# Performance work log

Measured on AMD Instinct MI355X. Metric: run time of the kernel, lower is better.

The kernel has to match this reference:

```python
import jax, jax.numpy as jnp
import numpy as np

B, T, ENC_IN, DEC_IN, U = 32768, 7, 60, 36, 356


def setup_inputs() -> dict:
    key = jax.random.key(0)
    ks = jax.random.split(key, 12)
    s = 0.05  # small weight scale for numerical sanity
    return {
        "x_batch": jax.random.normal(ks[0], (B, T, ENC_IN), jnp.float32),
        "m_batch": jax.random.normal(ks[1], (B, T, DEC_IN), jnp.float32),
        "enc_kernel": jax.random.normal(ks[2], (ENC_IN, 4 * U), jnp.float32) * s,
        "enc_rec_kernel": jax.random.normal(ks[3], (U, 4 * U), jnp.float32) * s,
        "enc_bias": jnp.zeros((4 * U,), jnp.float32),
        "dec_kernel": jax.random.normal(ks[4], (DEC_IN, 4 * U), jnp.float32) * s,
        "dec_rec_kernel": jax.random.normal(ks[5], (U, 4 * U), jnp.float32) * s,
        "dec_bias": jnp.zeros((4 * U,), jnp.float32),
        "W_map": jax.random.normal(ks[6], (T * U, 768), jnp.float32) * s,
        "b_map": jnp.zeros((768,), jnp.float32),
        "W_deep1": jax.random.normal(ks[7], (768, 768), jnp.float32) * s,
        "b_deep1": jnp.zeros((768,), jnp.float32),
        "W_deep2": jax.random.normal(ks[8], (768, 768), jnp.float32) * s,
        "b_deep2": jnp.zeros((768,), jnp.float32),
        "W_out": jax.random.normal(ks[9], (768, 168), jnp.float32) * s,
        "b_out": jnp.zeros((168,), jnp.float32),
    }


def _lstm(x, K, R, b, h0, c0):
    """Keras-style LSTM. x: [B,T,D]. Returns (hs [B,T,U], h_T, c_T).
    Gate order i, f, g(candidate), o; sigmoid recurrent activation, tanh activation."""
    xz = jnp.einsum('btd,dg->btg', x, K) + b  # precompute input projections [B,T,4U]

    def step(carry, xz_t):
        h, c = carry
        z = xz_t + h @ R
        i, f, g, o = jnp.split(z, 4, axis=-1)
        c = jax.nn.sigmoid(f) * c + jax.nn.sigmoid(i) * jnp.tanh(g)
        h = jax.nn.sigmoid(o) * jnp.tanh(c)
        return (h, c), h

    (h, c), hs = jax.lax.scan(step, (h0, c0), jnp.swapaxes(xz, 0, 1))
    return jnp.swapaxes(hs, 0, 1), h, c


def reference(x_batch, m_batch, enc_kernel, enc_rec_kernel, enc_bias,
              dec_kernel, dec_rec_kernel, dec_bias,
              W_map, b_map, W_deep1, b_deep1, W_deep2, b_deep2, W_out, b_out):
    b = x_batch.shape[0]
    z = jnp.zeros((b, U), x_batch.dtype)
    # encoder: only final states used
    _, s_h, s_c = _lstm(x_batch, enc_kernel, enc_rec_kernel, enc_bias, z, z)
    # decoder: full sequence, initialized with encoder states
    decoded, _, _ = _lstm(m_batch, dec_kernel, dec_rec_kernel, dec_bias, s_h, s_c)
    f = decoded.reshape(b, -1)  # [B, 7*356]
    m = jax.nn.relu(f @ W_map + b_map)
    d = jnp.tanh(m @ W_deep1 + b_deep1)
    d = jnp.tanh(d @ W_deep2 + b_deep2)
    return d @ W_out + b_out
```

## Files before the change

kernel.cpp:

```cpp
#include <hip/hip_runtime.h>

typedef unsigned short u16;
typedef __attribute__((ext_vector_type(8))) short short8;
typedef __attribute__((ext_vector_type(4))) float f32x4;

#define B_ROWS 32768
#define T_STEPS 7
#define ENC_INd 60
#define DEC_INd 36
#define UNITS 356
#define KP_LSTM 448
#define H_OFF 64
#define HID 768
#define OUTN 168
#define OUTNP 256
#define KMAP 2688
#define HALF_E 44040192ull
#define WLSTM_E 688128

__device__ __forceinline__ u16 f2b(float f) {
  unsigned u = __builtin_bit_cast(unsigned, f);
  u += 0x7fffu + ((u >> 16) & 1u);
  return (u16)(u >> 16);
}
__device__ __forceinline__ float sigm(float x) { return 1.0f / (1.0f + __expf(-x)); }
__device__ __forceinline__ float tanhfast(float x) { return 2.0f / (1.0f + __expf(-2.0f * x)) - 1.0f; }

__global__ void fill_sentinel(float* __restrict__ out, int n, float v) {
  int i = blockIdx.x * 256 + threadIdx.x;
  int stride = gridDim.x * 256;
  for (; i < n; i += stride) out[i] = v;
}

__global__ void prep_lstm_w(const float* __restrict__ Km, const float* __restrict__ Rm,
                            const float* __restrict__ bias, int in_dim,
                            u16* __restrict__ WT, float* __restrict__ bias_r)
{
  int idx = blockIdx.x * 256 + threadIdx.x;
  if (idx >= WLSTM_E) return;
  int e    = idx & 7;
  int lane = (idx >> 3) & 63;
  int nf   = (idx >> 9) & 3;
  int t1   = idx >> 11;
  int kk   = t1 % 14;
  int g    = t1 / 14;
  int u = g * 16 + (lane & 15);
  int k = kk * 32 + ((lane >> 4) << 3) + e;
  float v = 0.f;
  if (u < UNITS) {
    int oc = nf * UNITS + u;
    if (k < in_dim) v = Km[(size_t)k * 1424 + oc];
    else if (k >= H_OFF && k < H_OFF + UNITS) v = Rm[(size_t)(k - H_OFF) * 1424 + oc];
    if (k == 0) bias_r[(u << 2) + nf] = bias[oc];
  } else if (k == 0) bias_r[(u << 2) + nf] = 0.f;
  WT[idx] = f2b(v);
}

__global__ void prep_map_w(const float* __restrict__ W, u16* __restrict__ WT)
{
  int idx = blockIdx.x * 256 + threadIdx.x;
  if (idx >= HID * KMAP) return;
  int n = idx / KMAP, k = idx - n * KMAP;
  int t = k / 384, kk = k - t * 384;
  float v = (kk < UNITS) ? W[(size_t)(t * UNITS + kk) * HID + n] : 0.f;
  WT[idx] = f2b(v);
}

__global__ void prep_mlp_w(const float* __restrict__ W, int korig, int norig, int kp,
                           u16* __restrict__ WT, int total)
{
  int idx = blockIdx.x * 256 + threadIdx.x;
  if (idx >= total) return;
  int n = idx / kp, k = idx - n * kp;
  float v = (k < korig && n < norig) ? W[(size_t)k * norig + n] : 0.f;
  WT[idx] = f2b(v);
}

__global__ __launch_bounds__(512)
void lstm_persistent(const float* __restrict__ xg, const float* __restrict__ mg,
                     const u16* __restrict__ WTe, const float* __restrict__ bre,
                     const u16* __restrict__ WTd, const float* __restrict__ brd,
                     u16* __restrict__ fbuf)
{
  __shared__ __align__(16) u16 A[32][KP_LSTM];

  const int tid = threadIdx.x;
  const int ns = tid >> 6;
  const int lane = tid & 63;
  const int l15 = lane & 15, l4 = lane >> 4;
  const int row0 = blockIdx.x * 32;

  float    c_reg[3][2][4];
  unsigned h_pack[3][2][2];
#pragma unroll
  for (int a = 0; a < 3; ++a)
#pragma unroll
    for (int b = 0; b < 2; ++b) {
      c_reg[a][b][0] = c_reg[a][b][1] = c_reg[a][b][2] = c_reg[a][b][3] = 0.f;
      h_pack[a][b][0] = 0u; h_pack[a][b][1] = 0u;
    }

#pragma unroll 1
  for (int s = 0; s < 14; ++s) {
    const u16*  wt = (s < 7) ? WTe : WTd;
    const float* br = (s < 7) ? bre : brd;
    const float* src = (s < 7) ? xg : mg;
    const int in_dim = (s < 7) ? ENC_INd : DEC_INd;
    const int t = (s < 7) ? s : s - 7;

    __syncthreads();

#pragma unroll
    for (int p = 0; p < 3; ++p) {
      const int g = p * 8 + ns;
      const int c = H_OFF + (g << 4) + l15;
      const int cb = c >> 3, ci = c & 7;
#pragma unroll
      for (int mf = 0; mf < 2; ++mf)
#pragma unroll
        for (int r = 0; r < 4; ++r) {
          const int row = (mf << 4) + (l4 << 2) + r;
          const int cbs = (cb & 56) | ((cb ^ row) & 7);
          unsigned pk = h_pack[p][mf][r >> 1];
          A[row][(cbs << 3) + ci] = (u16)((r & 1) ? (pk >> 16) : (pk & 0xffffu));
        }
    }
    if (tid < 256) {
      const int row = tid >> 3, cb = tid & 7;
      const float* sp = src + ((size_t)(row0 + row) * T_STEPS + t) * in_dim;
      const int cbs = cb ^ (row & 7);
      short8 vv;
#pragma unroll
      for (int j = 0; j < 8; ++j) {
        const int cc = (cb << 3) + j;
        float v = (cc < in_dim) ? sp[cc] : 0.f;
        vv[j] = (short)f2b(v);
      }
      *(short8*)&A[row][cbs << 3] = vv;
    }
    __syncthreads();

#pragma unroll 1
    for (int p = 0; p < 3; ++p) {
      const int g = p * 8 + ns;
      f32x4 acc[2][4] = {};
      const u16* bp = wt + ((size_t)g * 14) * 2048 + (lane << 3);

#pragma unroll 2
      for (int kk = 0; kk < 14; ++kk) {
        short8 af[2], bf[4];
#pragma unroll
        for (int mf = 0; mf < 2; ++mf) {
          const int ra = (mf << 4) + l15;
          const int cbA = (kk << 2) + l4;
          const int cbs = (cbA & 56) | ((cbA ^ ra) & 7);
          af[mf] = *(const short8*)&A[ra][cbs << 3];
        }
#pragma unroll
        for (int nf = 0; nf < 4; ++nf)
          bf[nf] = *(const short8*)(bp + kk * 2048 + (nf << 9));
#pragma unroll
        for (int mf = 0; mf < 2; ++mf)
#pragma unroll
          for (int nf = 0; nf < 4; ++nf)
            acc[mf][nf] = __builtin_amdgcn_mfma_f32_16x16x32_bf16(af[mf], bf[nf], acc[mf][nf], 0, 0, 0);
      }

      const int u = (g << 4) + l15;
      float bz[4];
#pragma unroll
      for (int nf = 0; nf < 4; ++nf) bz[nf] = br[(u << 2) + nf];
#pragma unroll
      for (int mf = 0; mf < 2; ++mf)
#pragma unroll
        for (int r = 0; r < 4; ++r) {
          const int row = (mf << 4) + (l4 << 2) + r;
          float zi = acc[mf][0][r] + bz[0];
          float zf = acc[mf][1][r] + bz[1];
          float zg = acc[mf][2][r] + bz[2];
          float zo = acc[mf][3][r] + bz[3];
          float ig = sigm(zi), fg = sigm(zf);
          float gg = tanhfast(zg), og = sigm(zo);
          float cn = fg * c_reg[p][mf][r] + ig * gg;
          c_reg[p][mf][r] = cn;
          float hv = og * tanhfast(cn);
          u16 hb = f2b(hv);
          unsigned& hp = h_pack[p][mf][r >> 1];
          if (r & 1) hp = (hp & 0xffffu) | ((unsigned)hb << 16);
          else       hp = (hp & 0xffff0000u) | (unsigned)hb;
          if (s >= 7) {
            const int grow = row0 + row;
            fbuf[(size_t)(grow >> 14) * HALF_E
                 + ((size_t)(grow & 16383) * T_STEPS + t) * 384 + u] = hb;
          }
        }
    }
  }
}

template<int MODE>
__global__ __launch_bounds__(256)
void mlp_gemm(const u16* __restrict__ A, int lda, int kp,
              const u16* __restrict__ WT, const float* __restrict__ bias, int nreal,
              u16* __restrict__ outb, float* __restrict__ outf, int ldo)
{
  __shared__ __align__(16) u16 lds_a[128 * 64];
  __shared__ __align__(16) u16 lds_b[128 * 64];
  const int tid = threadIdx.x;
  const int wid = tid >> 6, lane = tid & 63;
  const int wm = (wid >> 1) << 6, wn = (wid & 1) << 6;
  const int l15 = lane & 15, l4 = lane >> 4;
  const int r0 = tid >> 3, c8 = tid & 7;
  const size_t abase = (size_t)blockIdx.x * 128 * lda;
  const size_t bbase = (size_t)blockIdx.y * 128 * kp;

  f32x4 acc[4][4] = {};

  for (int kt = 0; kt < kp; kt += 64) {
#pragma unroll
    for (int p = 0; p < 4; ++p) {
      int r = r0 + p * 32;
      short8 va = *(const short8*)(A + abase + (size_t)r * lda + kt + (c8 << 3));
      *(short8*)&lds_a[(r << 6) + ((c8 ^ (r & 7)) << 3)] = va;
      short8 vb = *(const short8*)(WT + bbase + (size_t)r * kp + kt + (c8 << 3));
      *(short8*)&lds_b[(r << 6) + ((c8 ^ (r & 7)) << 3)] = vb;
    }
    __syncthreads();
#pragma unroll
    for (int kk = 0; kk < 2; ++kk) {
      short8 af[4], bfr[4];
#pragma unroll
      for (int mf = 0; mf < 4; ++mf) {
        int ra = wm + (mf << 4) + l15;
        int cb = (kk << 2) + l4;
        af[mf] = *(const short8*)&lds_a[(ra << 6) + ((cb ^ (ra & 7)) << 3)];
      }
#pragma unroll
      for (int nf = 0; nf < 4; ++nf) {
        int rb = wn + (nf << 4) + l15;
        int cb = (kk << 2) + l4;
        bfr[nf] = *(const short8*)&lds_b[(rb << 6) + ((cb ^ (rb & 7)) << 3)];
      }
#pragma unroll
      for (int mf = 0; mf < 4; ++mf)
#pragma unroll
        for (int nf = 0; nf < 4; ++nf)
          acc[mf][nf] = __builtin_amdgcn_mfma_f32_16x16x32_bf16(af[mf], bfr[nf], acc[mf][nf], 0, 0, 0);
    }
    __syncthreads();
  }

#pragma unroll
  for (int mf = 0; mf < 4; ++mf) {
    int rowb = blockIdx.x * 128 + wm + (mf << 4) + (l4 << 2);
#pragma unroll
    for (int r = 0; r < 4; ++r) {
      int row = rowb + r;
#pragma unroll
      for (int nf = 0; nf < 4; ++nf) {
        int n = blockIdx.y * 128 + wn + (nf << 4) + l15;
        float v = acc[mf][nf][r];
        size_t oi = (size_t)row * ldo + n;
        if (MODE == 3) {
          outb[oi] = f2b(tanhfast(v + bias[n]));
        } else if (MODE == 5) {
          outb[oi] = f2b(fmaxf(v + bias[n], 0.f));
        } else {
          if (n < nreal) outf[oi] = v + bias[n];
        }
      }
    }
  }
}

extern "C" void kernel_launch(void* const* d_in, const int* in_sizes, int n_in,
                              void* d_out, int out_size, void* d_ws, size_t ws_size,
                              hipStream_t stream)
{
  const float* x    = (const float*)d_in[0];
  const float* m    = (const float*)d_in[1];
  const float* ek   = (const float*)d_in[2];
  const float* erk  = (const float*)d_in[3];
  const float* eb   = (const float*)d_in[4];
  const float* dk   = (const float*)d_in[5];
  const float* drk  = (const float*)d_in[6];
  const float* dbi  = (const float*)d_in[7];
  const float* wmap = (const float*)d_in[8];
  const float* bmap = (const float*)d_in[9];
  const float* wd1  = (const float*)d_in[10];
  const float* bd1  = (const float*)d_in[11];
  const float* wd2  = (const float*)d_in[12];
  const float* bd2  = (const float*)d_in[13];
  const float* wout = (const float*)d_in[14];
  const float* bout = (const float*)d_in[15];

  char* ws = (char*)d_ws;
  size_t off = 0;
  auto alloc = [&](size_t bytes) { char* p = ws + off; off += (bytes + 255) & ~(size_t)255; return p; };

  u16*   WT_enc  = (u16*)  alloc((size_t)WLSTM_E * 2);
  u16*   WT_dec  = (u16*)  alloc((size_t)WLSTM_E * 2);
  float* b_enc_r = (float*)alloc((size_t)384 * 4 * 4);
  float* b_dec_r = (float*)alloc((size_t)384 * 4 * 4);
  u16*   WT_map  = (u16*)  alloc((size_t)HID * KMAP * 2);
  u16*   WT_d1   = (u16*)  alloc((size_t)HID * HID * 2);
  u16*   WT_d2   = (u16*)  alloc((size_t)HID * HID * 2);
  u16*   WT_out  = (u16*)  alloc((size_t)OUTNP * HID * 2);
  u16*   m1_h1   = (u16*)  alloc((size_t)16384 * HID * 2);
  u16*   fbuf    = (u16*)  alloc((size_t)2 * HALF_E * 2);
  const size_t NEED = off;

  if (ws_size < NEED) {
    fill_sentinel<<<256, 256, 0, stream>>>((float*)d_out, out_size, (float)(ws_size >> 20));
    return;
  }

  u16* fb_h0 = fbuf;
  u16* fb_h1 = fbuf + HALF_E;
  u16* m1_h0 = fb_h1;
  u16* m2_h0 = fb_h0;
  u16* m2_h1 = fb_h0 + (size_t)16384 * HID;
  u16* m3_h0 = fb_h1;
  u16* m3_h1 = m1_h1;

  prep_lstm_w<<<(WLSTM_E + 255) / 256, 256, 0, stream>>>(ek, erk, eb, ENC_INd, WT_enc, b_enc_r);
  prep_lstm_w<<<(WLSTM_E + 255) / 256, 256, 0, stream>>>(dk, drk, dbi, DEC_INd, WT_dec, b_dec_r);
  prep_map_w<<<((HID * KMAP) + 255) / 256, 256, 0, stream>>>(wmap, WT_map);
  prep_mlp_w<<<((HID * HID) + 255) / 256, 256, 0, stream>>>(wd1, HID, HID, HID, WT_d1, HID * HID);
  prep_mlp_w<<<((HID * HID) + 255) / 256, 256, 0, stream>>>(wd2, HID, HID, HID, WT_d2, HID * HID);
  prep_mlp_w<<<((OUTNP * HID) + 255) / 256, 256, 0, stream>>>(wout, HID, OUTN, HID, WT_out, OUTNP * HID);

  lstm_persistent<<<1024, 512, 0, stream>>>(x, m, WT_enc, b_enc_r, WT_dec, b_dec_r, fbuf);

  mlp_gemm<5><<<dim3(128, 6), 256, 0, stream>>>(fb_h1, KMAP, KMAP, WT_map, bmap, HID, m1_h1, nullptr, HID);
  mlp_gemm<5><<<dim3(128, 6), 256, 0, stream>>>(fb_h0, KMAP, KMAP, WT_map, bmap, HID, m1_h0, nullptr, HID);
  mlp_gemm<3><<<dim3(128, 6), 256, 0, stream>>>(m1_h0, HID, HID, WT_d1, bd1, HID, m2_h0, nullptr, HID);
  mlp_gemm<3><<<dim3(128, 6), 256, 0, stream>>>(m1_h1, HID, HID, WT_d1, bd1, HID, m2_h1, nullptr, HID);
  mlp_gemm<3><<<dim3(128, 6), 256, 0, stream>>>(m2_h0, HID, HID, WT_d2, bd2, HID, m3_h0, nullptr, HID);
  mlp_gemm<3><<<dim3(128, 6), 256, 0, stream>>>(m2_h1, HID, HID, WT_d2, bd2, HID, m3_h1, nullptr, HID);
  mlp_gemm<4><<<dim3(128, 2), 256, 0, stream>>>(m3_h0, HID, HID, WT_out, bout, OUTN,
                                                nullptr, (float*)d_out, OUTN);
  mlp_gemm<4><<<dim3(128, 2), 256, 0, stream>>>(m3_h1, HID, HID, WT_out, bout, OUTN,
                                                nullptr, (float*)d_out + (size_t)16384 * OUTN, OUTN);
}
```

Before: 1.530 ms.

## Double-buffer LSTM hidden-state LDS tile to drop one barrier per step

The LSTM tile in LDS is now double-buffered by step parity. Each new h value is written straight into the other buffer during the gate epilogue, so the register-packed h state, the separate scatter phase and the leading __syncthreads per step are gone. Both buffers are zeroed once up front so the first step sees h=0. This doubles the kernel's LDS footprint, which may lower occupancy, and the scattered 2-byte LDS stores now sit inside the epilogue.

```diff
diff --git a/kernel.cpp b/kernel.cpp
--- a/kernel.cpp
+++ b/kernel.cpp
@@ -82,7 +82,7 @@
                      const u16* __restrict__ WTd, const float* __restrict__ brd,
                      u16* __restrict__ fbuf)
 {
-  __shared__ __align__(16) u16 A[32][KP_LSTM];
+  __shared__ __align__(16) u16 A[2][32][KP_LSTM];
 
   const int tid = threadIdx.x;
   const int ns = tid >> 6;
@@ -90,15 +90,21 @@
   const int l15 = lane & 15, l4 = lane >> 4;
   const int row0 = blockIdx.x * 32;
 
-  float    c_reg[3][2][4];
-  unsigned h_pack[3][2][2];
+  float c_reg[3][2][4];
 #pragma unroll
   for (int a = 0; a < 3; ++a)
 #pragma unroll
-    for (int b = 0; b < 2; ++b) {
+    for (int b = 0; b < 2; ++b)
       c_reg[a][b][0] = c_reg[a][b][1] = c_reg[a][b][2] = c_reg[a][b][3] = 0.f;
-      h_pack[a][b][0] = 0u; h_pack[a][b][1] = 0u;
-    }
+
+  {
+    short8 z = {};
+    for (int q = tid; q < 2 * 32 * 48; q += 512) {
+      int buf = q / 1536, rem = q - buf * 1536;
+      int row = rem / 48, blk = 8 + (rem - row * 48);
+      *(short8*)&A[buf][row][blk << 3] = z;
+    }
+  }
 
 #pragma unroll 1
   for (int s = 0; s < 14; ++s) {
@@ -107,24 +113,8 @@
     const float* src = (s < 7) ? xg : mg;
     const int in_dim = (s < 7) ? ENC_INd : DEC_INd;
     const int t = (s < 7) ? s : s - 7;
-
-    __syncthreads();
-
-#pragma unroll
-    for (int p = 0; p < 3; ++p) {
-      const int g = p * 8 + ns;
-      const int c = H_OFF + (g << 4) + l15;
-      const int cb = c >> 3, ci = c & 7;
-#pragma unroll
-      for (int mf = 0; mf < 2; ++mf)
-#pragma unroll
-        for (int r = 0; r < 4; ++r) {
-          const int row = (mf << 4) + (l4 << 2) + r;
-          const int cbs = (cb & 56) | ((cb ^ row) & 7);
-          unsigned pk = h_pack[p][mf][r >> 1];
-          A[row][(cbs << 3) + ci] = (u16)((r & 1) ? (pk >> 16) : (pk & 0xffffu));
-        }
-    }
+    const int par = s & 1;
+
     if (tid < 256) {
       const int row = tid >> 3, cb = tid & 7;
       const float* sp = src + ((size_t)(row0 + row) * T_STEPS + t) * in_dim;
@@ -136,7 +126,7 @@
         float v = (cc < in_dim) ? sp[cc] : 0.f;
         vv[j] = (short)f2b(v);
       }
-      *(short8*)&A[row][cbs << 3] = vv;
+      *(short8*)&A[par][row][cbs << 3] = vv;
     }
     __syncthreads();
 
@@ -154,7 +144,7 @@
           const int ra = (mf << 4) + l15;
           const int cbA = (kk << 2) + l4;
           const int cbs = (cbA & 56) | ((cbA ^ ra) & 7);
-          af[mf] = *(const short8*)&A[ra][cbs << 3];
+          af[mf] = *(const short8*)&A[par][ra][cbs << 3];
         }
 #pragma unroll
         for (int nf = 0; nf < 4; ++nf)
@@ -167,6 +157,7 @@
       }
 
       const int u = (g << 4) + l15;
+      const int ch = H_OFF + u, cbh = ch >> 3, cih = ch & 7;
       float bz[4];
 #pragma unroll
       for (int nf = 0; nf < 4; ++nf) bz[nf] = br[(u << 2) + nf];
@@ -185,9 +176,8 @@
           c_reg[p][mf][r] = cn;
           float hv = og * tanhfast(cn);
           u16 hb = f2b(hv);
-          unsigned& hp = h_pack[p][mf][r >> 1];
-          if (r & 1) hp = (hp & 0xffffu) | ((unsigned)hb << 16);
-          else       hp = (hp & 0xffff0000u) | (unsigned)hb;
+          const int cbs = (cbh & 56) | ((cbh ^ row) & 7);
+          A[par ^ 1][row][(cbs << 3) + cih] = hb;
           if (s >= 7) {
             const int grow = row0 + row;
             fbuf[(size_t)(grow >> 14) * HALF_E
```

Measured after the change: 1.460 ms. 1.05x faster.
